# Kernel tuning notes

Hardware: AMD Instinct MI355X
Metric: run time of the kernel (lower is better)

## Reference

```python
import jax, jax.numpy as jnp
import numpy as np

E = 1024      # embed_dim
H = 16        # num_heads
D = E // H    # head_dim = 64
K = 4         # num_hyper_nodes
MAX_SEQ = 8192
ROPE_BASE = 10000.0
SCALE = D ** -0.5


def rotate_half(x):
    half = x.shape[-1] // 2
    return jnp.concatenate([-x[..., half:], x[..., :half]], axis=-1)


def _rope_cache():
    inv_freq = 1.0 / (ROPE_BASE ** (jnp.arange(0, D, 2, dtype=jnp.float32) / D))
    t = jnp.arange(MAX_SEQ, dtype=jnp.float32)
    freqs = jnp.outer(t, inv_freq)                       # (MAX_SEQ, D/2)
    emb = jnp.concatenate([freqs, freqs], axis=-1)       # (MAX_SEQ, D)
    return jnp.cos(emb), jnp.sin(emb)


def setup_inputs() -> dict:
    key = jax.random.key(0)
    ks = jax.random.split(key, 6)
    B, S = 2, 2048
    w_scale = E ** -0.5  # keep pre-softmax logits in a sane range
    return {
        "x":  jax.random.normal(ks[0], (B, S, E), dtype=jnp.float32),
        "Wq": jax.random.normal(ks[1], (E, E), dtype=jnp.float32) * w_scale,
        "Wk": jax.random.normal(ks[2], (E, E), dtype=jnp.float32) * w_scale,
        "Wv": jax.random.normal(ks[3], (E, E), dtype=jnp.float32) * w_scale,
        "Wr": jax.random.normal(ks[4], (E, H * K), dtype=jnp.float32) * w_scale,
        "Wo": jax.random.normal(ks[5], (E, E), dtype=jnp.float32) * w_scale,
    }


def reference(x, Wq, Wk, Wv, Wr, Wo):
    B, S, _ = x.shape
    # projections -> (B, H, S, D)
    q = (x @ Wq).reshape(B, S, H, D).transpose(0, 2, 1, 3)
    k = (x @ Wk).reshape(B, S, H, D).transpose(0, 2, 1, 3)
    v = (x @ Wv).reshape(B, S, H, D).transpose(0, 2, 1, 3)

    # node routing probabilities (B, H, S, K)
    logits = (x @ Wr).reshape(B, S, H, K).transpose(0, 2, 1, 3)
    node_probs = jax.nn.softmax(logits, axis=-1)

    # expected per-node position: sum_{j<i} p[j,k]  -> (B, H, S, K)
    expected_pos = jnp.cumsum(node_probs, axis=2) - node_probs

    # fractional-position RoPE via linear interpolation of the cos/sin cache
    cos_c, sin_c = _rope_cache()
    pos = jnp.clip(expected_pos, 0.0, MAX_SEQ - 1)
    pf = pos.astype(jnp.int32)                   # floor
    pc = jnp.minimum(pf + 1, MAX_SEQ - 1)        # ceil
    frac = (pos - pf.astype(pos.dtype))[..., None]
    cos = cos_c[pf] + frac * (cos_c[pc] - cos_c[pf])   # (B,H,S,K,D)
    sin = sin_c[pf] + frac * (sin_c[pc] - sin_c[pf])

    # Weighted combine over nodes. Since q_k = q*cos_k + rh(q)*sin_k is linear
    # in (cos_k, sin_k), sum_k p_k * q_k = q * (sum_k p_k cos_k) + rh(q) * (sum_k p_k sin_k)
    cos_w = jnp.einsum('bhsk,bhskd->bhsd', node_probs, cos)
    sin_w = jnp.einsum('bhsk,bhskd->bhsd', node_probs, sin)
    q_r = q * cos_w + rotate_half(q) * sin_w
    k_r = k * cos_w + rotate_half(k) * sin_w

    # P(same node) weights (B, H, S, S)
    node_w = jnp.einsum('bhik,bhjk->bhij', node_probs, node_probs)

    scores = jnp.einsum('bhid,bhjd->bhij', q_r, k_r) * SCALE
    scores = scores + jnp.log(node_w + 1e-8)
    causal = jnp.tril(jnp.ones((S, S), dtype=bool))
    scores = jnp.where(causal[None, None], scores, -jnp.inf)
    attn = jax.nn.softmax(scores, axis=-1)

    out = jnp.einsum('bhij,bhjd->bhid', attn, v)
    out = out.transpose(0, 2, 1, 3).reshape(B, S, E)
    return out @ Wo
```

## Files before the change

kernel.cpp:

```cpp
#include <hip/hip_runtime.h>

#define E_ 1024
#define H_ 16
#define D_ 64
#define K_ 4
#define S_ 2048
#define B_ 2
#define BS_ 4096
#define BH_ 32
#define CT_ 2080

typedef __attribute__((ext_vector_type(8))) short short8;
typedef __attribute__((ext_vector_type(4))) float f32x4;
typedef __attribute__((ext_vector_type(4))) unsigned short u16x4;

__device__ __forceinline__ unsigned short f2bf(float f) {
  union { float f; unsigned u; } v; v.f = f;
  unsigned r = v.u + 0x7FFFu + ((v.u >> 16) & 1u);
  return (unsigned short)(r >> 16);
}
__device__ __forceinline__ float bf2f(unsigned short u) {
  union { unsigned u; float f; } v; v.u = ((unsigned)u) << 16; return v.f;
}

typedef __attribute__((address_space(1))) const void gvoid;
typedef __attribute__((address_space(3))) void lvoid;
__device__ __forceinline__ void gload_lds16(const void* g, void* l) {
  __builtin_amdgcn_global_load_lds((gvoid*)g, (lvoid*)l, 16, 0, 0);
}

__device__ __forceinline__ short8 lds8(const unsigned short* base, int row, int chunk) {
  int off = row * 128 + (((chunk ^ (row & 7)) & 7) << 4);
  return *(const short8*)((const char*)base + off);
}

#define SWZ_(d) (((d) & 7) ^ (((d) >> 3) & 7))

__device__ __forceinline__ float redmax16(float v) {
  int iv = __float_as_int(v);
  v = fmaxf(v, __int_as_float(__builtin_amdgcn_update_dpp(iv, iv, 0xB1, 0xF, 0xF, true)));
  iv = __float_as_int(v);
  v = fmaxf(v, __int_as_float(__builtin_amdgcn_update_dpp(iv, iv, 0x4E, 0xF, 0xF, true)));
  v = fmaxf(v, __shfl_xor(v, 4, 16));
  v = fmaxf(v, __shfl_xor(v, 8, 16));
  return v;
}

__global__ __launch_bounds__(256) void k_convert_x(const float* __restrict__ x,
                                                   unsigned short* __restrict__ xb) {
  int i = blockIdx.x * 256 + threadIdx.x;
  float4 v = ((const float4*)x)[i];
  u16x4 o; o.x = f2bf(v.x); o.y = f2bf(v.y); o.z = f2bf(v.z); o.w = f2bf(v.w);
  ((u16x4*)xb)[i] = o;
}

__global__ __launch_bounds__(256) void k_transpose_w(const float* __restrict__ Wq,
    const float* __restrict__ Wk, const float* __restrict__ Wv, const float* __restrict__ Wo,
    unsigned short* __restrict__ wt) {
  const float* W = blockIdx.z == 0 ? Wq : blockIdx.z == 1 ? Wk : blockIdx.z == 2 ? Wv : Wo;
  unsigned short* out = wt + (size_t)blockIdx.z * E_ * E_;
  __shared__ float tile[64][65];
  int k0 = blockIdx.y * 64, n0 = blockIdx.x * 64;
  int r = threadIdx.x >> 2, q4 = threadIdx.x & 3;
#pragma unroll
  for (int q = 0; q < 4; q++) {
    int c4 = q4 + q * 4;
    float4 v = *(const float4*)&W[(size_t)(k0 + r) * E_ + n0 + c4 * 4];
    tile[r][c4 * 4 + 0] = v.x; tile[r][c4 * 4 + 1] = v.y;
    tile[r][c4 * 4 + 2] = v.z; tile[r][c4 * 4 + 3] = v.w;
  }
  __syncthreads();
#pragma unroll
  for (int q = 0; q < 4; q++) {
    int cb = (q4 + q * 4) * 4;
    u16x4 o;
    o.x = f2bf(tile[cb + 0][r]); o.y = f2bf(tile[cb + 1][r]);
    o.z = f2bf(tile[cb + 2][r]); o.w = f2bf(tile[cb + 3][r]);
    *(u16x4*)&out[(size_t)(n0 + r) * E_ + k0 + cb] = o;
  }
}

__global__ __launch_bounds__(256) void k_cache(float* __restrict__ cosc, float* __restrict__ sinc) {
  int i = blockIdx.x * 256 + threadIdx.x;
  if (i >= CT_ * 32) return;
  int tt = i >> 5, f = i & 31;
  float invf = __expf(-(float)(2 * f) * (9.210340371976184f / 64.f));
  float ang = (float)tt * invf;
  cosc[i] = cosf(ang); sinc[i] = sinf(ang);
}

__global__ __launch_bounds__(256) void k_router(const float* __restrict__ x,
    const float* __restrict__ Wr, float* __restrict__ logits) {
  int rowblk = blockIdx.x * 8;
  int c = threadIdx.x & 63, rg = threadIdx.x >> 6;
  __shared__ float xs[8][128];
  float acc0 = 0.f, acc1 = 0.f;
  for (int e0 = 0; e0 < E_; e0 += 128) {
    __syncthreads();
    int idx = threadIdx.x;
    float4 v = *(const float4*)&x[(size_t)(rowblk + (idx >> 5)) * E_ + e0 + (idx & 31) * 4];
    *(float4*)&xs[idx >> 5][(idx & 31) * 4] = v;
    __syncthreads();
#pragma unroll 8
    for (int e = 0; e < 128; e++) {
      float w = Wr[(size_t)(e0 + e) * 64 + c];
      acc0 = fmaf(xs[rg * 2 + 0][e], w, acc0);
      acc1 = fmaf(xs[rg * 2 + 1][e], w, acc1);
    }
  }
  logits[(size_t)(rowblk + rg * 2 + 0) * 64 + c] = acc0;
  logits[(size_t)(rowblk + rg * 2 + 1) * 64 + c] = acc1;
}

__global__ __launch_bounds__(256) void k_scan(const float* __restrict__ logits,
    float* __restrict__ probs, unsigned short* __restrict__ pb, float* __restrict__ epos) {
  int bh = blockIdx.x; int b = bh >> 4, h = bh & 15;
  int t = threadIdx.x;
  float p[8][4];
  float own[4] = {0.f, 0.f, 0.f, 0.f};
#pragma unroll
  for (int r = 0; r < 8; r++) {
    int s = t * 8 + r;
    float4 lg = *(const float4*)&logits[(size_t)(b * S_ + s) * 64 + h * 4];
    float m = fmaxf(fmaxf(lg.x, lg.y), fmaxf(lg.z, lg.w));
    float e0 = __expf(lg.x - m), e1 = __expf(lg.y - m), e2 = __expf(lg.z - m), e3 = __expf(lg.w - m);
    float inv = 1.f / (e0 + e1 + e2 + e3);
    p[r][0] = e0 * inv; p[r][1] = e1 * inv; p[r][2] = e2 * inv; p[r][3] = e3 * inv;
    own[0] += p[r][0]; own[1] += p[r][1]; own[2] += p[r][2]; own[3] += p[r][3];
    float4 pv; pv.x = p[r][0]; pv.y = p[r][1]; pv.z = p[r][2]; pv.w = p[r][3];
    *(float4*)&probs[((size_t)bh * S_ + s) * 4] = pv;
    u16x4 pu; pu.x = f2bf(p[r][0]); pu.y = f2bf(p[r][1]);
    pu.z = f2bf(p[r][2]); pu.w = f2bf(p[r][3]);
    *(u16x4*)&pb[((size_t)bh * S_ + s) * 4] = pu;
  }
  __shared__ float sc[4][256];
#pragma unroll
  for (int k = 0; k < 4; k++) sc[k][t] = own[k];
  __syncthreads();
  for (int off = 1; off < 256; off <<= 1) {
    float v0 = 0, v1 = 0, v2 = 0, v3 = 0;
    if (t >= off) { v0 = sc[0][t - off]; v1 = sc[1][t - off]; v2 = sc[2][t - off]; v3 = sc[3][t - off]; }
    __syncthreads();
    if (t >= off) { sc[0][t] += v0; sc[1][t] += v1; sc[2][t] += v2; sc[3][t] += v3; }
    __syncthreads();
  }
  float run[4];
#pragma unroll
  for (int k = 0; k < 4; k++) run[k] = sc[k][t] - own[k];
#pragma unroll
  for (int r = 0; r < 8; r++) {
    int s = t * 8 + r;
    float4 ev; ev.x = run[0]; ev.y = run[1]; ev.z = run[2]; ev.w = run[3];
    *(float4*)&epos[((size_t)bh * S_ + s) * 4] = ev;
    run[0] += p[r][0]; run[1] += p[r][1]; run[2] += p[r][2]; run[3] += p[r][3];
  }
}

__global__ __launch_bounds__(256) void k_cwsw(const float* __restrict__ probs,
    const float* __restrict__ epos, const float* __restrict__ cosc, const float* __restrict__ sinc,
    float* __restrict__ cw, float* __restrict__ sw) {
  int bh = blockIdx.y;
  int s = blockIdx.x * 8 + (threadIdx.x >> 5);
  int f = threadIdx.x & 31;
  size_t row = (size_t)bh * S_ + s;
  float cacc = 0.f, sacc = 0.f;
#pragma unroll
  for (int k = 0; k < 4; k++) {
    float pk = probs[row * 4 + k];
    float pos = epos[row * 4 + k];
    pos = fminf(fmaxf(pos, 0.f), (float)(CT_ - 2));
    int pf = (int)pos; float fr = pos - (float)pf;
    float c0 = cosc[pf * 32 + f], c1 = cosc[pf * 32 + 32 + f];
    float s0 = sinc[pf * 32 + f], s1 = sinc[pf * 32 + 32 + f];
    cacc = fmaf(pk, c0 + fr * (c1 - c0), cacc);
    sacc = fmaf(pk, s0 + fr * (s1 - s0), sacc);
  }
  cw[row * 32 + f] = cacc; sw[row * 32 + f] = sacc;
}

__device__ __forceinline__ void gemm_128x128(const unsigned short* __restrict__ A,
    const unsigned short* __restrict__ Bt, int m0, int n0,
    unsigned short* lA, unsigned short* lB, f32x4 acc[4][4]) {
  int t = threadIdx.x, w = t >> 6, lane = t & 63;
  int wm = w >> 1, wn = w & 1;
  int arow = lane & 15, agrp = lane >> 4;
  for (int k0 = 0; k0 < E_; k0 += 64) {
    __syncthreads();
#pragma unroll
    for (int j = 0; j < 4; j++) {
      int c = j * 256 + w * 64 + lane;
      int row = c >> 3, slot = c & 7;
      gload_lds16(A + (size_t)(m0 + row) * E_ + k0 + ((slot ^ (row & 7)) << 3),
                  lA + (size_t)(j * 256 + w * 64) * 8);
      gload_lds16(Bt + (size_t)(n0 + row) * E_ + k0 + ((slot ^ (row & 7)) << 3),
                  lB + (size_t)(j * 256 + w * 64) * 8);
    }
    __syncthreads();
#pragma unroll
    for (int ks = 0; ks < 2; ks++) {
      short8 af[4], bfr[4];
#pragma unroll
      for (int mi = 0; mi < 4; mi++) af[mi] = lds8(lA, wm * 64 + mi * 16 + arow, ks * 4 + agrp);
#pragma unroll
      for (int nj = 0; nj < 4; nj++) bfr[nj] = lds8(lB, wn * 64 + nj * 16 + arow, ks * 4 + agrp);
#pragma unroll
      for (int mi = 0; mi < 4; mi++)
#pragma unroll
        for (int nj = 0; nj < 4; nj++)
          acc[mi][nj] = __builtin_amdgcn_mfma_f32_16x16x32_bf16(af[mi], bfr[nj], acc[mi][nj], 0, 0, 0);
    }
  }
}

__global__ __launch_bounds__(256) void k_gemm_qkv(const unsigned short* __restrict__ xb,
    const unsigned short* __restrict__ wt, const float* __restrict__ cw, const float* __restrict__ sw,
    unsigned short* __restrict__ qr, unsigned short* __restrict__ kr, unsigned short* __restrict__ vb) {
  __shared__ unsigned short lA[128 * 64], lB[128 * 64];
  int z = blockIdx.z;
  int m0 = blockIdx.y * 128, n0 = blockIdx.x * 128;
  f32x4 acc[4][4];
  f32x4 zero4 = {0.f, 0.f, 0.f, 0.f};
#pragma unroll
  for (int a = 0; a < 4; a++)
#pragma unroll
    for (int b2 = 0; b2 < 4; b2++) acc[a][b2] = zero4;
  gemm_128x128(xb, wt + (size_t)z * E_ * E_, m0, n0, lA, lB, acc);

  int t = threadIdx.x, w = t >> 6, lane = t & 63;
  int wm = w >> 1, wn = w & 1;
  int arow = lane & 15, agrp = lane >> 4;
  if (z == 2) {
#pragma unroll
    for (int mi = 0; mi < 4; mi++)
#pragma unroll
      for (int reg = 0; reg < 4; reg++) {
        int i = m0 + wm * 64 + mi * 16 + agrp * 4 + reg;
        int b = i >> 11, s = i & 2047;
#pragma unroll
        for (int nj = 0; nj < 4; nj++) {
          int col = n0 + wn * 64 + nj * 16 + arow;
          int h = col >> 6, d = col & 63;
          vb[((size_t)(b * H_ + h) * S_ + s) * 64 + d] = f2bf(acc[mi][nj][reg]);
        }
      }
  } else {
    unsigned short* out = (z == 0) ? qr : kr;
    float scl = (z == 0) ? 0.18033688011f : 1.0f;
    int h = (n0 + wn * 64) >> 6;
#pragma unroll
    for (int mi = 0; mi < 4; mi++)
#pragma unroll
      for (int reg = 0; reg < 4; reg++) {
        int i = m0 + wm * 64 + mi * 16 + agrp * 4 + reg;
        int b = i >> 11, s = i & 2047;
        size_t rbase = (size_t)(b * H_ + h) * S_ + s;
        float cw0 = cw[rbase * 32 + arow], cw1 = cw[rbase * 32 + 16 + arow];
        float sw0 = sw[rbase * 32 + arow], sw1 = sw[rbase * 32 + 16 + arow];
#pragma unroll
        for (int nj = 0; nj < 4; nj++) {
          float v = acc[mi][nj][reg];
          float part = acc[mi][nj ^ 2][reg];
          float rh = (nj < 2) ? -part : part;
          float cwv = (nj & 1) ? cw1 : cw0;
          float swv = (nj & 1) ? sw1 : sw0;
          out[rbase * 64 + nj * 16 + arow] = f2bf((v * cwv + rh * swv) * scl);
        }
      }
  }
}

__global__ __launch_bounds__(256) void k_gemm_out(const unsigned short* __restrict__ ob,
    const unsigned short* __restrict__ wot, float* __restrict__ dout) {
  __shared__ unsigned short lA[64 * 64];
  __shared__ unsigned short lB[128 * 64];
  int m0 = blockIdx.y * 64, n0 = blockIdx.x * 128;
  int t = threadIdx.x, w = t >> 6, lane = t & 63;
  int arow = lane & 15, agrp = lane >> 4;
  f32x4 acc[4][2];
  f32x4 zero4 = {0.f, 0.f, 0.f, 0.f};
#pragma unroll
  for (int a = 0; a < 4; a++) { acc[a][0] = zero4; acc[a][1] = zero4; }
  for (int k0 = 0; k0 < E_; k0 += 64) {
    __syncthreads();
#pragma unroll
    for (int j = 0; j < 2; j++) {
      int c = j * 256 + t;
      int row = c >> 3, slot = c & 7;
      gload_lds16(ob + (size_t)(m0 + row) * E_ + k0 + ((slot ^ (row & 7)) << 3),
                  lA + (size_t)c * 8);
    }
#pragma unroll
    for (int j = 0; j < 4; j++) {
      int c = j * 256 + t;
      int row = c >> 3, slot = c & 7;
      gload_lds16(wot + (size_t)(n0 + row) * E_ + k0 + ((slot ^ (row & 7)) << 3),
                  lB + (size_t)c * 8);
    }
    __syncthreads();
#pragma unroll
    for (int ks = 0; ks < 2; ks++) {
      short8 af[4], bfr[2];
#pragma unroll
      for (int mi = 0; mi < 4; mi++) af[mi] = lds8(lA, mi * 16 + arow, ks * 4 + agrp);
#pragma unroll
      for (int nj = 0; nj < 2; nj++) bfr[nj] = lds8(lB, w * 32 + nj * 16 + arow, ks * 4 + agrp);
#pragma unroll
      for (int mi = 0; mi < 4; mi++)
#pragma unroll
        for (int nj = 0; nj < 2; nj++)
          acc[mi][nj] = __builtin_amdgcn_mfma_f32_16x16x32_bf16(af[mi], bfr[nj], acc[mi][nj], 0, 0, 0);
    }
  }
#pragma unroll
  for (int mi = 0; mi < 4; mi++)
#pragma unroll
    for (int reg = 0; reg < 4; reg++) {
      int i = m0 + mi * 16 + agrp * 4 + reg;
#pragma unroll
      for (int nj = 0; nj < 2; nj++) {
        int col = n0 + w * 32 + nj * 16 + arow;
        dout[(size_t)i * E_ + col] = acc[mi][nj][reg];
      }
    }
}

__device__ const int4 kChunk[38] = {
  { 8,0, 8, 8},{ 8,9,17, 9},{12,0, 8,19},{12,9,17,20},
  { 7,0, 7, 6},{ 7,8,15, 7},{10,0, 7,13},{11,0, 7,16},{11,8,15,17},{11,16,23,18},
  {12,18,25,21},{14,0, 7,26},{14,8,15,27},{15,0, 7,30},{15,8,15,31},{15,16,23,32},
  {15,24,31,33},{ 3,0, 7,-1},
  { 6,0, 6, 4},{ 6,7,13, 5},{ 9,0, 6,10},{ 9,7,13,11},{10,8,14,14},{10,15,21,15},
  {13,0, 6,22},{13,7,13,23},{13,14,20,24},{13,21,27,25},{14,16,22,28},{14,23,29,29},
  { 5,0, 5, 2},{ 5,6,11, 3},{ 9,14,19,12},{ 2,0, 5,-1},
  { 4,0, 4, 0},{ 4,5, 9, 1},{ 1,0, 3,-1},{ 0,0, 1,-1}
};

__device__ __forceinline__ void qk_phase(const unsigned short* lKc, const short8 qf[2][2],
                                         int arow, int agrp, f32x4 sacc[2][4]) {
#pragma unroll
  for (int ks = 0; ks < 2; ks++)
#pragma unroll
    for (int ct = 0; ct < 4; ct++) {
      short8 kf = lds8(lKc, ct * 16 + arow, ks * 4 + agrp);
      sacc[0][ct] = __builtin_amdgcn_mfma_f32_16x16x32_bf16(qf[0][ks], kf, sacc[0][ct], 0, 0, 0);
      sacc[1][ct] = __builtin_amdgcn_mfma_f32_16x16x32_bf16(qf[1][ks], kf, sacc[1][ct], 0, 0, 0);
    }
}

__device__ __forceinline__ void softmax_half(const f32x4 sacc[4], const short8 piF,
    const short8 pjF[4], unsigned short* lPh, int kv0, int ig_base, int arow, int agrp,
    float mrow[4], f32x4 oacc[4], f32x4& o4) {
  f32x4 eps4 = {1e-8f, 1e-8f, 1e-8f, 1e-8f};
  f32x4 nwa[4];
#pragma unroll
  for (int ct = 0; ct < 4; ct++)
    nwa[ct] = __builtin_amdgcn_mfma_f32_16x16x32_bf16(piF, pjF[ct], eps4, 0, 0, 0);
  float sv[4][4];
  float rmax[4] = {-1e30f, -1e30f, -1e30f, -1e30f};
  if (kv0 + 63 > ig_base) {
#pragma unroll
    for (int ct = 0; ct < 4; ct++) {
      int jg = kv0 + ct * 16 + arow;
#pragma unroll
      for (int reg = 0; reg < 4; reg++) {
        int ig = ig_base + agrp * 4 + reg;
        float xv = sacc[ct][reg];
        if (jg > ig) xv = -1e30f;
        sv[ct][reg] = xv;
        rmax[reg] = fmaxf(rmax[reg], xv);
      }
    }
  } else {
#pragma unroll
    for (int ct = 0; ct < 4; ct++)
#pragma unroll
      for (int reg = 0; reg < 4; reg++) {
        float xv = sacc[ct][reg];
        sv[ct][reg] = xv;
        rmax[reg] = fmaxf(rmax[reg], xv);
      }
  }
#pragma unroll
  for (int reg = 0; reg < 4; reg++) rmax[reg] = redmax16(rmax[reg]);
  bool ok = (rmax[0] <= mrow[0] + 11.5f) & (rmax[1] <= mrow[1] + 11.5f) &
            (rmax[2] <= mrow[2] + 11.5f) & (rmax[3] <= mrow[3] + 11.5f);
  if (!__all(ok)) {
    float alpha[4];
#pragma unroll
    for (int reg = 0; reg < 4; reg++) {
      float mn = fmaxf(mrow[reg], rmax[reg]);
      alpha[reg] = __builtin_amdgcn_exp2f(mrow[reg] - mn);
      mrow[reg] = mn;
    }
#pragma unroll
    for (int dt = 0; dt < 4; dt++) {
      f32x4 o = oacc[dt];
      o.x *= alpha[0]; o.y *= alpha[1]; o.z *= alpha[2]; o.w *= alpha[3];
      oacc[dt] = o;
    }
    o4.x *= alpha[0]; o4.y *= alpha[1]; o4.z *= alpha[2]; o4.w *= alpha[3];
  }
#pragma unroll
  for (int ct = 0; ct < 4; ct++)
#pragma unroll
    for (int reg = 0; reg < 4; reg++) {
      float p = __builtin_amdgcn_exp2f(sv[ct][reg] - mrow[reg]) * nwa[ct][reg];
      int row = agrp * 4 + reg, col = ct * 16 + arow;
      int off = row * 128 + ((col * 2) ^ ((row & 7) << 4));
      *(unsigned short*)((char*)lPh + off) = f2bf(p);
    }
}

__device__ __forceinline__ void pv_phase(const unsigned short* lP0, const unsigned short* lP1,
    const unsigned short* lVc, int arow, int agrp, f32x4 oacc0[4], f32x4 oacc1[4],
    f32x4& o40, f32x4& o41) {
  const short8 ones = {16256, 16256, 16256, 16256, 16256, 16256, 16256, 16256};
#pragma unroll
  for (int ks = 0; ks < 2; ks++) {
    short8 pf0 = lds8(lP0, arow, ks * 4 + agrp);
    short8 pf1 = lds8(lP1, arow, ks * 4 + agrp);
    o40 = __builtin_amdgcn_mfma_f32_16x16x32_bf16(pf0, ones, o40, 0, 0, 0);
    o41 = __builtin_amdgcn_mfma_f32_16x16x32_bf16(pf1, ones, o41, 0, 0, 0);
#pragma unroll
    for (int dt = 0; dt < 4; dt++) {
      int d = dt * 16 + arow;
      int off = d * 128 + ((((ks * 4 + agrp)) ^ SWZ_(d)) << 4);
      short8 vf = *(const short8*)((const char*)lVc + off);
      oacc0[dt] = __builtin_amdgcn_mfma_f32_16x16x32_bf16(pf0, vf, oacc0[dt], 0, 0, 0);
      oacc1[dt] = __builtin_amdgcn_mfma_f32_16x16x32_bf16(pf1, vf, oacc1[dt], 0, 0, 0);
    }
  }
}

__global__ __launch_bounds__(256, 2) void k_attn(const unsigned short* __restrict__ qr,
    const unsigned short* __restrict__ kr, const unsigned short* __restrict__ vb,
    const unsigned short* __restrict__ pb, unsigned short* __restrict__ ob,
    unsigned short* __restrict__ ObP, float* __restrict__ ml) {
  __shared__ unsigned short lK[2][64 * 64];
  __shared__ unsigned short lV[2][64 * 64];
  __shared__ unsigned short lP[4][2][16 * 64];
  int id = blockIdx.x;
  int xcd = id & 7, slt = id >> 3;
  int bh = xcd * 4 + (slt & 3);
  int4 ck = kChunk[slt >> 2];
  int qt2 = ck.x, j0 = ck.y, j1 = ck.z, part = ck.w;
  int t = threadIdx.x, w = t >> 6, lane = t & 63;
  int arow = lane & 15, agrp = lane >> 4;
  int q0 = qt2 * 128;
  size_t base = (size_t)bh * S_ * 64;
  size_t bhS = (size_t)bh * S_;

  short8 qf[2][2];
  short8 piF[2];
  float mrow[2][4];
  f32x4 oacc[2][4];
  f32x4 o4[2];
  f32x4 zero4 = {0.f, 0.f, 0.f, 0.f};
#pragma unroll
  for (int hh = 0; hh < 2; hh++) {
#pragma unroll
    for (int ks = 0; ks < 2; ks++)
      qf[hh][ks] = *(const short8*)&qr[base + (size_t)(q0 + hh * 64 + w * 16 + arow) * 64 + ks * 32 + agrp * 8];
    u16x4 pv = {0, 0, 0, 0};
    if (agrp == 0) pv = *(const u16x4*)&pb[(bhS + q0 + hh * 64 + w * 16 + arow) * 4];
    short8 z = {0, 0, 0, 0, 0, 0, 0, 0};
    z[0] = (short)pv.x; z[1] = (short)pv.y; z[2] = (short)pv.z; z[3] = (short)pv.w;
    piF[hh] = z;
#pragma unroll
    for (int reg = 0; reg < 4; reg++) mrow[hh][reg] = -1e30f;
#pragma unroll
    for (int dt = 0; dt < 4; dt++) oacc[hh][dt] = zero4;
    o4[hh] = zero4;
  }

  auto stageK = [&](int jt, int buf) {
#pragma unroll
    for (int j = 0; j < 2; j++) {
      int c = j * 256 + w * 64 + lane;
      int row = c >> 3, slot = c & 7;
      gload_lds16(kr + base + (size_t)(jt * 64 + row) * 64 + ((slot ^ (row & 7)) << 3),
                  &lK[buf][(size_t)(j * 256 + w * 64) * 8]);
    }
  };
  auto loadV = [&](int jt, short8 vr[2]) {
#pragma unroll
    for (int j = 0; j < 2; j++) {
      int c = j * 256 + t;
      int row = c >> 3, d0 = (c & 7) * 8;
      vr[j] = *(const short8*)&vb[base + (size_t)(jt * 64 + row) * 64 + d0];
    }
  };
  auto scatterV = [&](const short8 vr[2], int buf) {
#pragma unroll
    for (int j = 0; j < 2; j++) {
      int c = j * 256 + t;
      int row = c >> 3, d0 = (c & 7) * 8;
#pragma unroll
      for (int x = 0; x < 8; x++) {
        int d = d0 + x;
        int off = d * 128 + ((row * 2) ^ (SWZ_(d) << 4));
        *(unsigned short*)((char*)&lV[buf][0] + off) = (unsigned short)vr[j][x];
      }
    }
  };
  auto loadPj = [&](int jt, u16x4 pj[4]) {
#pragma unroll
    for (int ct = 0; ct < 4; ct++) {
      u16x4 z = {0, 0, 0, 0};
      if (agrp == 0) z = *(const u16x4*)&pb[(bhS + jt * 64 + ct * 16 + arow) * 4];
      pj[ct] = z;
    }
  };

  short8 vreg[2];
  u16x4 pjv[4], pjvn[4];
  loadV(j0, vreg);
  stageK(j0, 0);
  scatterV(vreg, 0);
  loadPj(j0, pjv);
  __syncthreads();

  int nt = j1 - j0 + 1;
  for (int i = 0; i < nt; i++) {
    int cur = i & 1;
    int kv0 = (j0 + i) * 64;
    bool hn = (i + 1) < nt;
    if (hn) {
      loadV(j0 + i + 1, vreg);
      stageK(j0 + i + 1, cur ^ 1);
    }

    f32x4 sacc[2][4];
#pragma unroll
    for (int hh = 0; hh < 2; hh++)
#pragma unroll
      for (int ct = 0; ct < 4; ct++) sacc[hh][ct] = zero4;

    __builtin_amdgcn_s_setprio(1);
    qk_phase(&lK[cur][0], qf, arow, agrp, sacc);
    __builtin_amdgcn_s_setprio(0);

    short8 pjF[4];
#pragma unroll
    for (int ct = 0; ct < 4; ct++) {
      short8 z = {0, 0, 0, 0, 0, 0, 0, 0};
      z[0] = (short)pjv[ct].x; z[1] = (short)pjv[ct].y;
      z[2] = (short)pjv[ct].z; z[3] = (short)pjv[ct].w;
      pjF[ct] = z;
    }
#pragma unroll
    for (int hh = 0; hh < 2; hh++)
      softmax_half(sacc[hh], piF[hh], pjF, &lP[w][hh][0], kv0, q0 + hh * 64 + w * 16,
                   arow, agrp, mrow[hh], oacc[hh], o4[hh]);

    if (hn) {
      scatterV(vreg, cur ^ 1);
      loadPj(j0 + i + 1, pjvn);
    }

    asm volatile("s_waitcnt lgkmcnt(0)" ::: "memory");
    __builtin_amdgcn_sched_barrier(0);
    __builtin_amdgcn_s_setprio(1);
    pv_phase(&lP[w][0][0], &lP[w][1][0], &lV[cur][0], arow, agrp, oacc[0], oacc[1],
             o4[0], o4[1]);
    __builtin_amdgcn_s_setprio(0);
    if (hn) {
#pragma unroll
      for (int ct = 0; ct < 4; ct++) pjv[ct] = pjvn[ct];
    }
    __syncthreads();
  }

  if (part >= 0) {
    unsigned short* Op = ObP + ((size_t)bh * 34 + part) * 8192;
    float* mlp = ml + ((size_t)bh * 34 + part) * 256;
#pragma unroll
    for (int hh = 0; hh < 2; hh++) {
#pragma unroll
      for (int dt = 0; dt < 4; dt++)
#pragma unroll
        for (int reg = 0; reg < 4; reg++) {
          int row = hh * 64 + w * 16 + agrp * 4 + reg;
          Op[row * 64 + dt * 16 + arow] = f2bf(oacc[hh][dt][reg]);
        }
      if (arow == 0) {
#pragma unroll
        for (int reg = 0; reg < 4; reg++) {
          int row = hh * 64 + w * 16 + agrp * 4 + reg;
          mlp[row] = mrow[hh][reg];
          mlp[128 + row] = o4[hh][reg];
        }
      }
    }
  } else {
    int b = bh >> 4, h8 = bh & 15;
#pragma unroll
    for (int hh = 0; hh < 2; hh++) {
      f32x4 inv4;
      inv4.x = 1.f / o4[hh].x; inv4.y = 1.f / o4[hh].y;
      inv4.z = 1.f / o4[hh].z; inv4.w = 1.f / o4[hh].w;
#pragma unroll
      for (int dt = 0; dt < 4; dt++)
#pragma unroll
        for (int reg = 0; reg < 4; reg++) {
          int i = q0 + hh * 64 + w * 16 + agrp * 4 + reg;
          int d = dt * 16 + arow;
          float v = oacc[hh][dt][reg] * inv4[reg];
          ob[((size_t)(b * S_ + i) * H_ + h8) * 64 + d] = f2bf(v);
        }
    }
  }
}

__global__ __launch_bounds__(256) void k_merge(const unsigned short* __restrict__ ObP,
    const float* __restrict__ ml, unsigned short* __restrict__ ob) {
  int qx = blockIdx.x, bh = blockIdx.y;
  int qt2 = 4 + qx;
  int np = qt2 <= 8 ? 2 : (qt2 <= 12 ? 3 : 4);
  int bslot = qt2 <= 8 ? (qt2 - 4) * 2 : (qt2 <= 12 ? 10 + (qt2 - 9) * 3 : 22 + (qt2 - 13) * 4);
  int t = threadIdx.x;
  int r = t >> 1, dh = (t & 1) * 32;
  float mp[4], lp[4];
  float m = -1e30f;
  for (int p2 = 0; p2 < np; p2++) {
    const float* mlp = ml + ((size_t)bh * 34 + bslot + p2) * 256;
    mp[p2] = mlp[r]; lp[p2] = mlp[128 + r];
    m = fmaxf(m, mp[p2]);
  }
  float a[4], l = 0.f;
  for (int p2 = 0; p2 < np; p2++) { a[p2] = __builtin_amdgcn_exp2f(mp[p2] - m); l = fmaf(lp[p2], a[p2], l); }
  float inv = 1.f / l;
  for (int p2 = 0; p2 < np; p2++) a[p2] *= inv;
  int i = qt2 * 128 + r, b = bh >> 4, h = bh & 15;
  unsigned short* op = ob + ((size_t)(b * S_ + i) * H_ + h) * 64 + dh;
#pragma unroll
  for (int q = 0; q < 8; q++) {
    float a0 = 0.f, a1 = 0.f, a2 = 0.f, a3 = 0.f;
    for (int p2 = 0; p2 < np; p2++) {
      const unsigned short* Op = ObP + ((size_t)bh * 34 + bslot + p2) * 8192 + r * 64 + dh + q * 4;
      u16x4 xx = *(const u16x4*)Op;
      a0 = fmaf(bf2f(xx.x), a[p2], a0);
      a1 = fmaf(bf2f(xx.y), a[p2], a1);
      a2 = fmaf(bf2f(xx.z), a[p2], a2);
      a3 = fmaf(bf2f(xx.w), a[p2], a3);
    }
    u16x4 o; o.x = f2bf(a0); o.y = f2bf(a1); o.z = f2bf(a2); o.w = f2bf(a3);
    *(u16x4*)(op + q * 4) = o;
  }
}

extern "C" void kernel_launch(void* const* d_in, const int* in_sizes, int n_in,
                              void* d_out, int out_size, void* d_ws, size_t ws_size,
                              hipStream_t stream) {
  const float* x  = (const float*)d_in[0];
  const float* Wq = (const float*)d_in[1];
  const float* Wk = (const float*)d_in[2];
  const float* Wv = (const float*)d_in[3];
  const float* Wr = (const float*)d_in[4];
  const float* Wo = (const float*)d_in[5];
  float* dout = (float*)d_out;

  char* p = (char*)d_ws;
  auto alloc = [&](size_t bytes) -> char* {
    char* r = p; p += (bytes + 255) & ~(size_t)255; return r;
  };
  unsigned short* xb   = (unsigned short*)alloc((size_t)BS_ * E_ * 2);
  unsigned short* wt   = (unsigned short*)alloc((size_t)4 * E_ * E_ * 2);
  float* cosc          = (float*)alloc((size_t)CT_ * 32 * 4);
  float* sinc          = (float*)alloc((size_t)CT_ * 32 * 4);
  float* probs         = (float*)alloc((size_t)BH_ * S_ * 4 * 4);
  unsigned short* pb   = (unsigned short*)alloc((size_t)BH_ * S_ * 4 * 2);
  float* logits        = (float*)alloc((size_t)BS_ * 64 * 4);
  float* epos          = (float*)alloc((size_t)BH_ * S_ * 4 * 4);
  float* cw            = (float*)alloc((size_t)BH_ * S_ * 32 * 4);
  float* sw            = (float*)alloc((size_t)BH_ * S_ * 32 * 4);
  unsigned short* qrb  = (unsigned short*)alloc((size_t)BH_ * S_ * 64 * 2);
  unsigned short* krb  = (unsigned short*)alloc((size_t)BH_ * S_ * 64 * 2);
  unsigned short* vbb  = (unsigned short*)alloc((size_t)BH_ * S_ * 64 * 2);
  unsigned short* obb  = (unsigned short*)alloc((size_t)BS_ * E_ * 2);
  if ((size_t)(p - (char*)d_ws) > ws_size) return;

  unsigned short* ObP = (unsigned short*)logits;
  float* mlbuf = (float*)xb;

  k_convert_x<<<BS_ * E_ / 4 / 256, 256, 0, stream>>>(x, xb);
  k_transpose_w<<<dim3(16, 16, 4), 256, 0, stream>>>(Wq, Wk, Wv, Wo, wt);
  k_cache<<<(CT_ * 32 + 255) / 256, 256, 0, stream>>>(cosc, sinc);
  k_router<<<BS_ / 8, 256, 0, stream>>>(x, Wr, logits);
  k_scan<<<BH_, 256, 0, stream>>>(logits, probs, pb, epos);
  k_cwsw<<<dim3(S_ / 8, BH_), 256, 0, stream>>>(probs, epos, cosc, sinc, cw, sw);
  k_gemm_qkv<<<dim3(8, 32, 3), 256, 0, stream>>>(xb, wt, cw, sw, qrb, krb, vbb);
  k_attn<<<dim3(38 * BH_), 256, 0, stream>>>(qrb, krb, vbb, pb, obb, ObP, mlbuf);
  k_merge<<<dim3(12, BH_), 256, 0, stream>>>(ObP, mlbuf, obb);
  k_gemm_out<<<dim3(8, 64), 256, 0, stream>>>(obb, wt + (size_t)3 * E_ * E_, dout);
}
```

Measured before the change: 210.8 us.

## Store V transposed from projection and stage it via direct global-to-LDS loads

The QKV projection epilogue now writes V in a transposed (b,h,d,s) layout with 4-element vector stores. The attention kernel can then stage V tiles with direct global-to-LDS async loads using the same swizzle as K, in place of register loads followed by 16 scalar LDS scatter stores per thread. Separately, the softmax P write now packs bf16 pairs with v_cvt_pk_bf16_f32 instead of per-element manual rounding. The transposed layout trades contiguous-row V stores for strided ones in the projection epilogue.

```diff
diff --git a/kernel.cpp b/kernel.cpp
--- a/kernel.cpp
+++ b/kernel.cpp
@@ -33,8 +33,6 @@
   int off = row * 128 + (((chunk ^ (row & 7)) & 7) << 4);
   return *(const short8*)((const char*)base + off);
 }
-
-#define SWZ_(d) (((d) & 7) ^ (((d) >> 3) & 7))
 
 __device__ __forceinline__ float redmax16(float v) {
   int iv = __float_as_int(v);
@@ -231,18 +229,19 @@
   int arow = lane & 15, agrp = lane >> 4;
   if (z == 2) {
 #pragma unroll
-    for (int mi = 0; mi < 4; mi++)
-#pragma unroll
-      for (int reg = 0; reg < 4; reg++) {
-        int i = m0 + wm * 64 + mi * 16 + agrp * 4 + reg;
-        int b = i >> 11, s = i & 2047;
-#pragma unroll
-        for (int nj = 0; nj < 4; nj++) {
-          int col = n0 + wn * 64 + nj * 16 + arow;
-          int h = col >> 6, d = col & 63;
-          vb[((size_t)(b * H_ + h) * S_ + s) * 64 + d] = f2bf(acc[mi][nj][reg]);
-        }
+    for (int mi = 0; mi < 4; mi++) {
+      int i0 = m0 + wm * 64 + mi * 16 + agrp * 4;
+      int b = i0 >> 11, s0 = i0 & 2047;
+#pragma unroll
+      for (int nj = 0; nj < 4; nj++) {
+        int col = n0 + wn * 64 + nj * 16 + arow;
+        int h = col >> 6, dl = col & 63;
+        u16x4 o;
+        o.x = f2bf(acc[mi][nj][0]); o.y = f2bf(acc[mi][nj][1]);
+        o.z = f2bf(acc[mi][nj][2]); o.w = f2bf(acc[mi][nj][3]);
+        *(u16x4*)&vb[((size_t)(b * H_ + h) * 64 + dl) * S_ + s0] = o;
       }
+    }
   } else {
     unsigned short* out = (z == 0) ? qr : kr;
     float scl = (z == 0) ? 0.18033688011f : 1.0f;
@@ -403,12 +402,20 @@
 #pragma unroll
   for (int ct = 0; ct < 4; ct++)
 #pragma unroll
-    for (int reg = 0; reg < 4; reg++) {
-      float p = __builtin_amdgcn_exp2f(sv[ct][reg] - mrow[reg]) * nwa[ct][reg];
-      int row = agrp * 4 + reg, col = ct * 16 + arow;
-      int off = row * 128 + ((col * 2) ^ ((row & 7) << 4));
-      *(unsigned short*)((char*)lPh + off) = f2bf(p);
-    }
+    for (int reg = 0; reg < 4; reg++)
+      sv[ct][reg] = __builtin_amdgcn_exp2f(sv[ct][reg] - mrow[reg]) * nwa[ct][reg];
+#pragma unroll
+  for (int ct = 0; ct < 4; ct++) {
+    int col2 = (ct * 16 + arow) * 2;
+#pragma unroll
+    for (int rp = 0; rp < 2; rp++) {
+      unsigned pk;
+      asm("v_cvt_pk_bf16_f32 %0, %1, %2" : "=v"(pk) : "v"(sv[ct][rp * 2]), "v"(sv[ct][rp * 2 + 1]));
+      int r0 = agrp * 4 + rp * 2, r1 = r0 + 1;
+      *(unsigned short*)((char*)lPh + r0 * 128 + (col2 ^ ((r0 & 7) << 4))) = (unsigned short)pk;
+      *(unsigned short*)((char*)lPh + r1 * 128 + (col2 ^ ((r1 & 7) << 4))) = (unsigned short)(pk >> 16);
+    }
+  }
 }
 
 __device__ __forceinline__ void pv_phase(const unsigned short* lP0, const unsigned short* lP1,
@@ -423,9 +430,7 @@
     o41 = __builtin_amdgcn_mfma_f32_16x16x32_bf16(pf1, ones, o41, 0, 0, 0);
 #pragma unroll
     for (int dt = 0; dt < 4; dt++) {
-      int d = dt * 16 + arow;
-      int off = d * 128 + ((((ks * 4 + agrp)) ^ SWZ_(d)) << 4);
-      short8 vf = *(const short8*)((const char*)lVc + off);
+      short8 vf = lds8(lVc, dt * 16 + arow, ks * 4 + agrp);
       oacc0[dt] = __builtin_amdgcn_mfma_f32_16x16x32_bf16(pf0, vf, oacc0[dt], 0, 0, 0);
       oacc1[dt] = __builtin_amdgcn_mfma_f32_16x16x32_bf16(pf1, vf, oacc1[dt], 0, 0, 0);
     }
@@ -482,25 +487,13 @@
                   &lK[buf][(size_t)(j * 256 + w * 64) * 8]);
     }
   };
-  auto loadV = [&](int jt, short8 vr[2]) {
+  auto stageV = [&](int jt, int buf) {
 #pragma unroll
     for (int j = 0; j < 2; j++) {
-      int c = j * 256 + t;
-      int row = c >> 3, d0 = (c & 7) * 8;
-      vr[j] = *(const short8*)&vb[base + (size_t)(jt * 64 + row) * 64 + d0];
-    }
-  };
-  auto scatterV = [&](const short8 vr[2], int buf) {
-#pragma unroll
-    for (int j = 0; j < 2; j++) {
-      int c = j * 256 + t;
-      int row = c >> 3, d0 = (c & 7) * 8;
-#pragma unroll
-      for (int x = 0; x < 8; x++) {
-        int d = d0 + x;
-        int off = d * 128 + ((row * 2) ^ (SWZ_(d) << 4));
-        *(unsigned short*)((char*)&lV[buf][0] + off) = (unsigned short)vr[j][x];
-      }
+      int c = j * 256 + w * 64 + lane;
+      int row = c >> 3, slot = c & 7;
+      gload_lds16(vb + base + (size_t)row * S_ + jt * 64 + ((slot ^ (row & 7)) << 3),
+                  &lV[buf][(size_t)(j * 256 + w * 64) * 8]);
     }
   };
   auto loadPj = [&](int jt, u16x4 pj[4]) {
@@ -512,11 +505,9 @@
     }
   };
 
-  short8 vreg[2];
   u16x4 pjv[4], pjvn[4];
-  loadV(j0, vreg);
   stageK(j0, 0);
-  scatterV(vreg, 0);
+  stageV(j0, 0);
   loadPj(j0, pjv);
   __syncthreads();
 
@@ -526,8 +517,8 @@
     int kv0 = (j0 + i) * 64;
     bool hn = (i + 1) < nt;
     if (hn) {
-      loadV(j0 + i + 1, vreg);
       stageK(j0 + i + 1, cur ^ 1);
+      stageV(j0 + i + 1, cur ^ 1);
     }
 
     f32x4 sacc[2][4];
@@ -553,10 +544,7 @@
       softmax_half(sacc[hh], piF[hh], pjF, &lP[w][hh][0], kv0, q0 + hh * 64 + w * 16,
                    arow, agrp, mrow[hh], oacc[hh], o4[hh]);
 
-    if (hn) {
-      scatterV(vreg, cur ^ 1);
-      loadPj(j0 + i + 1, pjvn);
-    }
+    if (hn) loadPj(j0 + i + 1, pjvn);
 
     asm volatile("s_waitcnt lgkmcnt(0)" ::: "memory");
     __builtin_amdgcn_sched_barrier(0);
```

Measured after the change: 208.7 us. Within noise of the previous version (-1.0%).
